# Performance work log

Hardware: AMD Instinct MI355X
Metric: run time of the kernel (lower is better)

## Reference

```python
import jax, jax.numpy as jnp
import numpy as np

NUM_USERS = 4096
NUM_ITEMS = 8192
EMBED_DIM = 64
NUM_LAYERS = 3


def setup_inputs() -> dict:
    key = jax.random.key(0)
    k1, k2 = jax.random.split(key)
    # embedding table for users+items (nn.Embedding init normal std=0.1)
    x = jax.random.normal(k1, (NUM_USERS + NUM_ITEMS, EMBED_DIM), dtype=jnp.float32) * 0.1
    # dense 0/1 user-item interaction matrix (forward applies torch.nonzero to it)
    edge_index = jax.random.randint(k2, (NUM_USERS, NUM_ITEMS), 0, 2, dtype=jnp.int32)
    return {"x": x, "edge_index": edge_index}


def reference(x, edge_index):
    U, I, L = NUM_USERS, NUM_ITEMS, NUM_LAYERS
    adj = edge_index.astype(jnp.float32)  # [U, I], 0/1
    # symmetric degree normalization: adj / sqrt(deg_u * deg_i), nan (0/0) -> 0
    deg_u = jnp.sum(adj, axis=1)  # [U]
    deg_i = jnp.sum(adj, axis=0)  # [I]
    denom = jnp.sqrt(deg_u[:, None] * deg_i[None, :])  # [U, I]
    weights = jnp.where(denom > 0, adj / jnp.where(denom > 0, denom, 1.0), 0.0)
    # weights is identical every layer (depends only on edge_index)
    acc = jnp.zeros_like(x)
    for _ in range(L):
        # NOTE: original code concatenates (item-side, user-side) in this order
        x = jnp.concatenate([weights.T @ x[:U], weights @ x[U:]], axis=0)  # [I+U, d]
        acc = acc + x
    # alpha = 1/(1+L) * ones applied to every layer output
    return acc / (1.0 + L)
```

## Files before the change

### kernel.cpp

```cpp
#include <hip/hip_runtime.h>

#define NU 4096
#define NI 8192
#define ND 64
#define NTOT 12288
#define CT 8
#define CB 16
#define BROW 520

#define DSC 0.5f

typedef unsigned short u16;
typedef unsigned int u32;
typedef unsigned long long u64;

__device__ __forceinline__ u16 f2bf(float f) {
    union { float f; u32 u; } v; v.f = f;
    u32 u = v.u;
    u += 0x7FFFu + ((u >> 16) & 1u);
    return (u16)(u >> 16);
}

typedef short frag8 __attribute__((ext_vector_type(8)));
typedef float f32x4 __attribute__((ext_vector_type(4)));

__global__ __launch_bounds__(256) void k_pack2(const int* __restrict__ edge,
        u64* __restrict__ Apk, u64* __restrict__ ATpk) {
    __shared__ __align__(16) u16 At[256][40];
    __shared__ __align__(16) u64 Tt[512][6];
    const int t = threadIdx.x;
    const int u0 = (blockIdx.x >> 4) * 256;
    const int i0 = (blockIdx.x & 15) * 512;
    const int cg = t & 31;
    const int rb = t >> 5;

    #pragma unroll 4
    for (int rr = 0; rr < 32; rr++) {
        const int row = rb * 32 + rr;
        const int4* p = (const int4*)(edge + (size_t)(u0 + row) * NI + i0 + cg * 16);
        u32 bits = 0;
        #pragma unroll
        for (int m = 0; m < 4; m++) {
            int4 v = p[m];
            bits |= (v.x != 0 ? 1u : 0u) << (m * 4 + 0);
            bits |= (v.y != 0 ? 1u : 0u) << (m * 4 + 1);
            bits |= (v.z != 0 ? 1u : 0u) << (m * 4 + 2);
            bits |= (v.w != 0 ? 1u : 0u) << (m * 4 + 3);
        }
        At[row][cg] = (u16)bits;
    }
    __syncthreads();

    {
        u64* dst = Apk + (size_t)(u0 + t) * 128 + (i0 >> 6);
        #pragma unroll
        for (int q = 0; q < 4; q++) {
            uint4 v = *(const uint4*)&At[t][q * 8];
            *(uint4*)(dst + q * 2) = v;
        }
    }

    {
        const int lane = t & 63, w = t >> 6;
        const u64 M[6] = {0x00000000FFFFFFFFULL, 0x0000FFFF0000FFFFULL,
                          0x00FF00FF00FF00FFULL, 0x0F0F0F0F0F0F0F0FULL,
                          0x3333333333333333ULL, 0x5555555555555555ULL};
        #pragma unroll
        for (int sc = 0; sc < 8; sc++) {
            u64 x = *(const u64*)&At[w * 64 + lane][sc * 4];
            #pragma unroll
            for (int si = 0; si < 6; si++) {
                const int s = 32 >> si;
                u64 y = __shfl_xor(x, s, 64);
                x = (lane & s) ? ((x & ~M[si]) | ((y >> s) & M[si]))
                               : ((x &  M[si]) | ((y << s) & ~M[si]));
            }
            Tt[sc * 64 + lane][w] = x;
        }
    }
    __syncthreads();
    #pragma unroll
    for (int j = 0; j < 2; j++) {
        const int item = t * 2 + j;
        ulonglong2 a = *(const ulonglong2*)&Tt[item][0];
        ulonglong2 b = *(const ulonglong2*)&Tt[item][2];
        u64* dst = ATpk + (size_t)(i0 + item) * 64 + (u0 >> 6);
        *(ulonglong2*)dst = a;
        *(ulonglong2*)(dst + 2) = b;
    }
}

__global__ __launch_bounds__(256) void k_scale0(const float* __restrict__ x,
        const u64* __restrict__ Apk, const u64* __restrict__ ATpk,
        float* __restrict__ dsu, float* __restrict__ dsi,
        u16* __restrict__ BuT, u16* __restrict__ BiT) {
    __shared__ float sc[64];
    const int t = threadIdx.x;
    const int r0 = blockIdx.x * 64;
    {
        const int rl = t >> 2, part = t & 3;
        int cnt = 0;
        if (r0 < NU) {
            const u64* p = Apk + (size_t)(r0 + rl) * 128 + part * 32;
            #pragma unroll
            for (int i = 0; i < 32; i++) cnt += (int)__popcll(p[i]);
        } else {
            const u64* p = ATpk + (size_t)(r0 - NU + rl) * 64 + part * 16;
            #pragma unroll
            for (int i = 0; i < 16; i++) cnt += (int)__popcll(p[i]);
        }
        cnt += __shfl_xor(cnt, 1, 64);
        cnt += __shfl_xor(cnt, 2, 64);
        if (part == 0) {
            float s = cnt > 0 ? rsqrtf((float)cnt) : 0.f;
            sc[rl] = s;
            if (r0 < NU) dsu[r0 + rl] = s; else dsi[r0 - NU + rl] = s;
        }
    }
    __syncthreads();
    const int r4 = t >> 4, c4 = t & 15;
    float y[4][4];
    #pragma unroll
    for (int j = 0; j < 4; j++) {
        const int rl = r4 * 4 + j;
        const float s = sc[rl] * DSC;
        float4 xv = *(const float4*)(x + (size_t)(r0 + rl) * ND + c4 * 4);
        y[j][0] = xv.x * s; y[j][1] = xv.y * s;
        y[j][2] = xv.z * s; y[j][3] = xv.w * s;
    }
    u16* dst; size_t stride; int col0;
    if (r0 < NU) { dst = BuT; stride = NU; col0 = r0; }
    else         { dst = BiT; stride = NI; col0 = r0 - NU; }
    #pragma unroll
    for (int k = 0; k < 4; k++) {
        ushort4 w;
        w.x = f2bf(y[0][k]); w.y = f2bf(y[1][k]);
        w.z = f2bf(y[2][k]); w.w = f2bf(y[3][k]);
        *(ushort4*)(dst + (size_t)(c4 * 4 + k) * stride + col0 + r4 * 4) = w;
    }
}

__global__ __launch_bounds__(256, 2) void k_gemm(
        const u64* __restrict__ Apk, const u64* __restrict__ ATpk,
        const u16* __restrict__ BuT, const u16* __restrict__ BiT,
        float* __restrict__ Ptop, float* __restrict__ Pbot) {
    __shared__ __align__(16) u16 Bs[64 * BROW];
    const int t = threadIdx.x, bx = blockIdx.x;
    const int lane = t & 63, w = t >> 6, lr = lane & 15, lg = lane >> 4;
    const u64* abase; const u16* dense; int Kstr, wpr, kbase, pstr; float* Pout;
    if (bx < 256) {
        const int tile = bx >> 3, chunk = bx & 7;
        abase = ATpk + (size_t)(tile * 256) * 64 + chunk * 8; wpr = 64;
        dense = BuT; Kstr = NU; kbase = chunk * 512; pstr = CT * 64;
        Pout = Ptop + (size_t)(tile * 256) * pstr + chunk * 64;
    } else {
        const int b2 = bx - 256, tile = b2 >> 4, chunk = b2 & 15;
        abase = Apk + (size_t)(tile * 256) * 128 + chunk * 8; wpr = 128;
        dense = BiT; Kstr = NI; kbase = chunk * 512; pstr = CB * 64;
        Pout = Pbot + (size_t)(tile * 256) * pstr + chunk * 64;
    }
    const u16* gsrc = dense + kbase;
    #pragma unroll
    for (int it = 0; it < 16; it++) {
        const int e = it * 4 + w;
        __builtin_amdgcn_global_load_lds(
            (const __attribute__((address_space(1))) void*)
                (gsrc + (size_t)e * Kstr + lane * 8),
            (__attribute__((address_space(3))) void*)(&Bs[e * BROW]),
            16, 0, 0);
    }
    u64 aw[4][8];
    #pragma unroll
    for (int g = 0; g < 4; g++) {
        const u64* myrow = abase + (size_t)(w * 64 + g * 16 + lr) * wpr;
        #pragma unroll
        for (int q = 0; q < 4; q++) {
            ulonglong2 v = *(const ulonglong2*)(myrow + q * 2);
            aw[g][q * 2] = v.x; aw[g][q * 2 + 1] = v.y;
        }
    }
    f32x4 acc[4][4];
    #pragma unroll
    for (int g = 0; g < 4; g++)
        #pragma unroll
        for (int nt = 0; nt < 4; nt++) acc[g][nt] = f32x4{0.f, 0.f, 0.f, 0.f};
    __syncthreads();

    const int sh = lg * 8;
    #pragma unroll
    for (int kk = 0; kk < 8; kk++) {
        #pragma unroll
        for (int half = 0; half < 2; half++) {
            frag8 bf[4];
            #pragma unroll
            for (int g = 0; g < 4; g++) {
                const u32 b = (u32)(aw[g][kk] >> (sh + half * 32)) & 0xFFu;
                const u64 p = (u64)b * 0x20004000ULL;
                union { frag8 f; u32 u[4]; } bb;
                bb.u[0] = ((u32)(p     )) & 0x40004000u;
                bb.u[1] = ((u32)(p >> 2)) & 0x40004000u;
                bb.u[2] = ((u32)(p >> 4)) & 0x40004000u;
                bb.u[3] = ((u32)(p >> 6)) & 0x40004000u;
                bf[g] = bb.f;
            }
            #pragma unroll
            for (int nt = 0; nt < 4; nt++) {
                frag8 a = *(const frag8*)
                    &Bs[(nt * 16 + lr) * BROW + kk * 64 + half * 32 + sh];
                #pragma unroll
                for (int g = 0; g < 4; g++)
                    acc[g][nt] = __builtin_amdgcn_mfma_f32_16x16x32_bf16(
                        a, bf[g], acc[g][nt], 0, 0, 0);
            }
        }
    }
    __syncthreads();
    float* Fs = (float*)Bs;
    #pragma unroll
    for (int g = 0; g < 4; g++) {
        const int il = w * 64 + g * 16 + lr;
        #pragma unroll
        for (int nt = 0; nt < 4; nt++) {
            const int gr = nt * 4 + lg;
            *(f32x4*)&Fs[il * 64 + (((gr + il) & 15) * 4)] = acc[g][nt];
        }
    }
    __syncthreads();
    #pragma unroll
    for (int ii = 0; ii < 16; ii++) {
        const int slot = t + ii * 256;
        const int row = slot >> 4, g = slot & 15;
        f32x4 v = *(const f32x4*)&Fs[row * 64 + (((g + row) & 15) * 4)];
        *(f32x4*)&Pout[(size_t)row * pstr + g * 4] = v;
    }
}

__global__ __launch_bounds__(256) void k_reduce(
        const float* __restrict__ Ptop, const float* __restrict__ Pbot,
        const float* __restrict__ dsu, const float* __restrict__ dsi,
        float* __restrict__ accbuf, u16* __restrict__ BuTn,
        u16* __restrict__ BiTn, float* __restrict__ out, int layer) {
    __shared__ u16 TB[64][24];
    const int t = threadIdx.x, bx = blockIdx.x;
    const int rl = t >> 4, e4 = t & 15;
    int grow; float so;
    float sx = 0.f, sy = 0.f, sz = 0.f, sw = 0.f;
    if (bx < 512) {
        grow = bx * 16 + rl;
        const float* p = Ptop + (size_t)grow * (CT * 64) + e4 * 4;
        #pragma unroll
        for (int c = 0; c < CT; c++) {
            float4 v = *(const float4*)(p + c * 64);
            sx += v.x; sy += v.y; sz += v.z; sw += v.w;
        }
        so = dsi[grow];
    } else {
        const int u = (bx - 512) * 16 + rl;
        grow = NI + u;
        const float* p = Pbot + (size_t)u * (CB * 64) + e4 * 4;
        #pragma unroll
        for (int c = 0; c < CB; c++) {
            float4 v = *(const float4*)(p + c * 64);
            sx += v.x; sy += v.y; sz += v.z; sw += v.w;
        }
        so = dsu[grow - NI];
    }
    float4 y;
    y.x = sx * so; y.y = sy * so; y.z = sz * so; y.w = sw * so;
    const size_t o = (size_t)grow * ND + e4 * 4;
    if (layer == 0) {
        *(float4*)(accbuf + o) = y;
    } else if (layer == 1) {
        float4 a = *(const float4*)(accbuf + o);
        a.x += y.x; a.y += y.y; a.z += y.z; a.w += y.w;
        *(float4*)(accbuf + o) = a;
    } else {
        float4 a = *(const float4*)(accbuf + o);
        a.x = (a.x + y.x) * 0.25f; a.y = (a.y + y.y) * 0.25f;
        a.z = (a.z + y.z) * 0.25f; a.w = (a.w + y.w) * 0.25f;
        *(float4*)(out + o) = a;
    }
    if (layer != 2) {
        const float fn = ((grow < NU) ? dsu[grow] : dsi[grow - NU]) * DSC;
        TB[e4 * 4 + 0][rl] = f2bf(y.x * fn);
        TB[e4 * 4 + 1][rl] = f2bf(y.y * fn);
        TB[e4 * 4 + 2][rl] = f2bf(y.z * fn);
        TB[e4 * 4 + 3][rl] = f2bf(y.w * fn);
        __syncthreads();
        if (t < 128) {
            const int e = t >> 1, h = t & 1;
            u16* dst; size_t stride; int col0;
            if (bx < 256)      { dst = BuTn; stride = NU; col0 = bx * 16; }
            else if (bx < 512) { dst = BiTn; stride = NI; col0 = bx * 16 - NU; }
            else               { dst = BiTn; stride = NI; col0 = (bx - 512) * 16 + NI - NU; }
            uint4 v = *(const uint4*)&TB[e][h * 8];
            *(uint4*)(dst + (size_t)e * stride + col0 + h * 8) = v;
        }
    }
}

extern "C" void kernel_launch(void* const* d_in, const int* in_sizes, int n_in,
                              void* d_out, int out_size, void* d_ws, size_t ws_size,
                              hipStream_t stream) {
    (void)in_sizes; (void)n_in; (void)out_size; (void)ws_size;
    const float* x    = (const float*)d_in[0];
    const int*   edge = (const int*)d_in[1];
    float* out = (float*)d_out;

    char* ws = (char*)d_ws;
    size_t off = 0;
    u64* Apk  = (u64*)(ws + off); off += (size_t)NU * (NI / 64) * 8;
    u64* ATpk = (u64*)(ws + off); off += (size_t)NI * (NU / 64) * 8;
    float* dsu = (float*)(ws + off); off += (size_t)NU * 4;
    float* dsi = (float*)(ws + off); off += (size_t)NI * 4;
    u16* BuT0 = (u16*)(ws + off); off += (size_t)ND * NU * 2;
    u16* BuT1 = (u16*)(ws + off); off += (size_t)ND * NU * 2;
    u16* BiT0 = (u16*)(ws + off); off += (size_t)ND * NI * 2;
    u16* BiT1 = (u16*)(ws + off); off += (size_t)ND * NI * 2;
    float* acc  = (float*)(ws + off); off += (size_t)NTOT * ND * 4;
    float* Ptop = (float*)(ws + off); off += (size_t)NI * CT * 64 * 4;
    float* Pbot = (float*)(ws + off); off += (size_t)NU * CB * 64 * 4;

    k_pack2<<<256, 256, 0, stream>>>(edge, Apk, ATpk);
    k_scale0<<<NTOT / 64, 256, 0, stream>>>(x, Apk, ATpk, dsu, dsi, BuT0, BiT0);

    k_gemm<<<512, 256, 0, stream>>>(Apk, ATpk, BuT0, BiT0, Ptop, Pbot);
    k_reduce<<<768, 256, 0, stream>>>(Ptop, Pbot, dsu, dsi, acc, BuT1, BiT1, out, 0);
    k_gemm<<<512, 256, 0, stream>>>(Apk, ATpk, BuT1, BiT1, Ptop, Pbot);
    k_reduce<<<768, 256, 0, stream>>>(Ptop, Pbot, dsu, dsi, acc, BuT0, BiT0, out, 1);
    k_gemm<<<512, 256, 0, stream>>>(Apk, ATpk, BuT0, BiT0, Ptop, Pbot);
    k_reduce<<<768, 256, 0, stream>>>(Ptop, Pbot, dsu, dsi, acc,
                                      (u16*)nullptr, (u16*)nullptr, out, 2);
}
```

Baseline: 273.0 us.

## Double GEMM K-chunk per block with intra-block two-wave K-split reduction

Each GEMM block now covers twice the K range (1024 instead of 512) using 512 threads. Wave pairs split the K range and sum their accumulators through LDS before writing out. This halves the number of partial-sum chunks (CT 8→4, CB 16→8) written to global memory and later read by the reduce kernel. In exchange, the LDS tile roughly doubles to about 132KB per block, so only one block fits per CU, and an extra LDS read-modify-write pass is added.

```diff
diff --git a/kernel.cpp b/kernel.cpp
--- a/kernel.cpp
+++ b/kernel.cpp
@@ -4,9 +4,9 @@
 #define NI 8192
 #define ND 64
 #define NTOT 12288
-#define CT 8
-#define CB 16
-#define BROW 520
+#define CT 4
+#define CB 8
+#define BROW 1032
 
 #define DSC 0.5f
 
@@ -140,39 +140,40 @@
     }
 }
 
-__global__ __launch_bounds__(256, 2) void k_gemm(
+__global__ __launch_bounds__(512, 2) void k_gemm(
         const u64* __restrict__ Apk, const u64* __restrict__ ATpk,
         const u16* __restrict__ BuT, const u16* __restrict__ BiT,
         float* __restrict__ Ptop, float* __restrict__ Pbot) {
     __shared__ __align__(16) u16 Bs[64 * BROW];
     const int t = threadIdx.x, bx = blockIdx.x;
     const int lane = t & 63, w = t >> 6, lr = lane & 15, lg = lane >> 4;
+    const int kh = w & 1, wq = w >> 1;
     const u64* abase; const u16* dense; int Kstr, wpr, kbase, pstr; float* Pout;
-    if (bx < 256) {
-        const int tile = bx >> 3, chunk = bx & 7;
-        abase = ATpk + (size_t)(tile * 256) * 64 + chunk * 8; wpr = 64;
-        dense = BuT; Kstr = NU; kbase = chunk * 512; pstr = CT * 64;
+    if (bx < 128) {
+        const int tile = bx >> 2, chunk = bx & 3;
+        abase = ATpk + (size_t)(tile * 256) * 64 + chunk * 16 + kh * 8; wpr = 64;
+        dense = BuT; Kstr = NU; kbase = chunk * 1024; pstr = CT * 64;
         Pout = Ptop + (size_t)(tile * 256) * pstr + chunk * 64;
     } else {
-        const int b2 = bx - 256, tile = b2 >> 4, chunk = b2 & 15;
-        abase = Apk + (size_t)(tile * 256) * 128 + chunk * 8; wpr = 128;
-        dense = BiT; Kstr = NI; kbase = chunk * 512; pstr = CB * 64;
+        const int b2 = bx - 128, tile = b2 >> 3, chunk = b2 & 7;
+        abase = Apk + (size_t)(tile * 256) * 128 + chunk * 16 + kh * 8; wpr = 128;
+        dense = BiT; Kstr = NI; kbase = chunk * 1024; pstr = CB * 64;
         Pout = Pbot + (size_t)(tile * 256) * pstr + chunk * 64;
     }
     const u16* gsrc = dense + kbase;
     #pragma unroll
     for (int it = 0; it < 16; it++) {
-        const int e = it * 4 + w;
+        const int e = it * 4 + wq;
         __builtin_amdgcn_global_load_lds(
             (const __attribute__((address_space(1))) void*)
-                (gsrc + (size_t)e * Kstr + lane * 8),
-            (__attribute__((address_space(3))) void*)(&Bs[e * BROW]),
+                (gsrc + (size_t)e * Kstr + kh * 512 + lane * 8),
+            (__attribute__((address_space(3))) void*)(&Bs[e * BROW + kh * 512]),
             16, 0, 0);
     }
     u64 aw[4][8];
     #pragma unroll
     for (int g = 0; g < 4; g++) {
-        const u64* myrow = abase + (size_t)(w * 64 + g * 16 + lr) * wpr;
+        const u64* myrow = abase + (size_t)(wq * 64 + g * 16 + lr) * wpr;
         #pragma unroll
         for (int q = 0; q < 4; q++) {
             ulonglong2 v = *(const ulonglong2*)(myrow + q * 2);
@@ -187,6 +188,7 @@
     __syncthreads();
 
     const int sh = lg * 8;
+    const int kW = kh * 512;
     #pragma unroll
     for (int kk = 0; kk < 8; kk++) {
         #pragma unroll
@@ -206,7 +208,7 @@
             #pragma unroll
             for (int nt = 0; nt < 4; nt++) {
                 frag8 a = *(const frag8*)
-                    &Bs[(nt * 16 + lr) * BROW + kk * 64 + half * 32 + sh];
+                    &Bs[(nt * 16 + lr) * BROW + kW + kk * 64 + half * 32 + sh];
                 #pragma unroll
                 for (int g = 0; g < 4; g++)
                     acc[g][nt] = __builtin_amdgcn_mfma_f32_16x16x32_bf16(
@@ -216,19 +218,35 @@
     }
     __syncthreads();
     float* Fs = (float*)Bs;
-    #pragma unroll
-    for (int g = 0; g < 4; g++) {
-        const int il = w * 64 + g * 16 + lr;
-        #pragma unroll
-        for (int nt = 0; nt < 4; nt++) {
-            const int gr = nt * 4 + lg;
-            *(f32x4*)&Fs[il * 64 + (((gr + il) & 15) * 4)] = acc[g][nt];
-        }
-    }
-    __syncthreads();
-    #pragma unroll
-    for (int ii = 0; ii < 16; ii++) {
-        const int slot = t + ii * 256;
+    if (kh) {
+        #pragma unroll
+        for (int g = 0; g < 4; g++) {
+            const int il = wq * 64 + g * 16 + lr;
+            #pragma unroll
+            for (int nt = 0; nt < 4; nt++) {
+                const int gr = nt * 4 + lg;
+                *(f32x4*)&Fs[il * 64 + (((gr + il) & 15) * 4)] = acc[g][nt];
+            }
+        }
+    }
+    __syncthreads();
+    if (!kh) {
+        #pragma unroll
+        for (int g = 0; g < 4; g++) {
+            const int il = wq * 64 + g * 16 + lr;
+            #pragma unroll
+            for (int nt = 0; nt < 4; nt++) {
+                const int gr = nt * 4 + lg;
+                f32x4 v = *(const f32x4*)&Fs[il * 64 + (((gr + il) & 15) * 4)];
+                v = v + acc[g][nt];
+                *(f32x4*)&Fs[il * 64 + (((gr + il) & 15) * 4)] = v;
+            }
+        }
+    }
+    __syncthreads();
+    #pragma unroll
+    for (int ii = 0; ii < 8; ii++) {
+        const int slot = t + ii * 512;
         const int row = slot >> 4, g = slot & 15;
         f32x4 v = *(const f32x4*)&Fs[row * 64 + (((g + row) & 15) * 4)];
         *(f32x4*)&Pout[(size_t)row * pstr + g * 4] = v;
@@ -324,11 +342,11 @@
     k_pack2<<<256, 256, 0, stream>>>(edge, Apk, ATpk);
     k_scale0<<<NTOT / 64, 256, 0, stream>>>(x, Apk, ATpk, dsu, dsi, BuT0, BiT0);
 
-    k_gemm<<<512, 256, 0, stream>>>(Apk, ATpk, BuT0, BiT0, Ptop, Pbot);
+    k_gemm<<<256, 512, 0, stream>>>(Apk, ATpk, BuT0, BiT0, Ptop, Pbot);
     k_reduce<<<768, 256, 0, stream>>>(Ptop, Pbot, dsu, dsi, acc, BuT1, BiT1, out, 0);
-    k_gemm<<<512, 256, 0, stream>>>(Apk, ATpk, BuT1, BiT1, Ptop, Pbot);
+    k_gemm<<<256, 512, 0, stream>>>(Apk, ATpk, BuT1, BiT1, Ptop, Pbot);
     k_reduce<<<768, 256, 0, stream>>>(Ptop, Pbot, dsu, dsi, acc, BuT0, BiT0, out, 1);
-    k_gemm<<<512, 256, 0, stream>>>(Apk, ATpk, BuT0, BiT0, Ptop, Pbot);
+    k_gemm<<<256, 512, 0, stream>>>(Apk, ATpk, BuT0, BiT0, Ptop, Pbot);
     k_reduce<<<768, 256, 0, stream>>>(Ptop, Pbot, dsu, dsi, acc,
                                       (u16*)nullptr, (u16*)nullptr, out, 2);
 }
```

Result: no change. 275.6 us (+0.9%).
